# Kernel optimization log

Hardware: AMD Instinct MI355X
Metric: run time of the kernel (lower is better)

The kernel has to match this reference:

```python
import jax, jax.numpy as jnp
import numpy as np

KW = float(np.sqrt(3.0 * 3.0 / np.pi))  # hard-coded tube-of-response kernel width
EXT = 200.0  # half-extent of the FOV in mm (size = 400 per axis)
NLOR = 50000
NVOX = 128


def _make_lors(key, n, ext):
    # endpoints on opposite faces along the dominant (first) axis of the permuted frame
    k1, k2 = jax.random.split(key)
    yz1 = jax.random.uniform(k1, (2, n), minval=-ext, maxval=ext)
    yz2 = jax.random.uniform(k2, (2, n), minval=-ext, maxval=ext)
    x1 = jnp.full((1, n), -ext, jnp.float32)
    x2 = jnp.full((1, n), ext, jnp.float32)
    return jnp.concatenate([x1, yz1, x2, yz2], axis=0)  # [6, n]


def setup_inputs() -> dict:
    key = jax.random.key(0)
    ks = jax.random.split(key, 8)
    return {
        "image": jax.random.normal(ks[0], (NVOX, NVOX, NVOX), jnp.float32),
        "grid": jnp.array([NVOX, NVOX, NVOX], jnp.int32),
        "center": jnp.zeros((3,), jnp.float32),
        "size": jnp.full((3,), 2.0 * EXT, jnp.float32),
        "xlors": _make_lors(ks[1], NLOR, EXT),
        "ylors": _make_lors(ks[2], NLOR, EXT),
        "zlors": _make_lors(ks[3], NLOR, EXT),
        "xproj": jax.random.uniform(ks[4], (NLOR,), jnp.float32),
        "yproj": jax.random.uniform(ks[5], (NLOR,), jnp.float32),
        "zproj": jax.random.uniform(ks[6], (NLOR,), jnp.float32),
    }


def _backproject(shape, grid, center, size, lors, proj, kw):
    # Tube-of-response backprojection: march slices along axis 0, deposit a
    # Gaussian footprint (3x3 window) around the line crossing in each slice.
    N0, N1, N2 = shape
    v = size / grid.astype(jnp.float32)          # voxel size [3]
    lo = center - 0.5 * size                     # FOV lower corner [3]
    x = lo[0] + (jnp.arange(N0, dtype=jnp.float32) + 0.5) * v[0]  # slice centers [K]
    p1, p2 = lors[:, :3], lors[:, 3:6]           # [N,3]
    d = p2 - p1
    t = (x[None, :] - p1[:, :1]) / d[:, :1]      # [N,K]
    y = p1[:, 1:2] + t * d[:, 1:2]               # [N,K]
    z = p1[:, 2:3] + t * d[:, 2:3]
    fy = (y - lo[1]) / v[1] - 0.5                # fractional voxel coords
    fz = (z - lo[2]) / v[2] - 0.5
    off = jnp.arange(-1, 2)
    iy = jnp.floor(fy).astype(jnp.int32)[..., None] + off   # [N,K,3]
    iz = jnp.floor(fz).astype(jnp.int32)[..., None] + off
    cy = lo[1] + (iy.astype(jnp.float32) + 0.5) * v[1]
    cz = lo[2] + (iz.astype(jnp.float32) + 0.5) * v[2]
    dy = cy - y[..., None]
    dz = cz - z[..., None]
    d2 = dy[:, :, :, None] ** 2 + dz[:, :, None, :] ** 2    # [N,K,3,3]
    w = jnp.exp(-0.5 * d2 / (kw * kw))
    ok = ((iy >= 0) & (iy < N1))[:, :, :, None] \
       & ((iz >= 0) & (iz < N2))[:, :, None, :] \
       & ((t >= 0.0) & (t <= 1.0))[:, :, None, None]
    w = jnp.where(ok, w, 0.0) * proj[:, None, None, None]
    iyc = jnp.clip(iy, 0, N1 - 1)
    izc = jnp.clip(iz, 0, N2 - 1)
    kk = jnp.arange(N0)[None, :, None, None]
    flat = (kk * N1 + iyc[:, :, :, None]) * N2 + izc[:, :, None, :]  # [N,K,3,3]
    vol = jnp.zeros(N0 * N1 * N2, jnp.float32).at[flat.ravel()].add(w.ravel())
    return vol.reshape(N0, N1, N2)


def _perm(a, p):
    return a[jnp.array(p)]


def reference(image, grid, center, size, xlors, ylors, zlors, xproj, yproj, zproj):
    shape = image.shape
    # z-dominant LORs: base frame
    bpz = _backproject(shape, grid, center, size, zlors.T, zproj, KW)
    # x-dominant LORs: frame permuted [2,0,1], result transposed back [1,2,0]
    px = (2, 0, 1)
    shx = tuple(shape[i] for i in px)
    bpx = _backproject(shx, _perm(grid, px), _perm(center, px), _perm(size, px),
                       xlors.T, xproj, KW)
    bpxt = jnp.transpose(bpx, (1, 2, 0))
    # y-dominant LORs: frame permuted [1,0,2], result transposed back [1,0,2]
    py = (1, 0, 2)
    shy = tuple(shape[i] for i in py)
    bpy = _backproject(shy, _perm(grid, py), _perm(center, py), _perm(size, py),
                       ylors.T, yproj, KW)
    bpyt = jnp.transpose(bpy, (1, 0, 2))
    return bpxt + bpyt + bpz
```

## Files before the change

### kernel.cpp

```cpp
#include <hip/hip_runtime.h>
#include <stdint.h>

#define NVOX 128
#define VOL  (NVOX * NVOX * NVOX)
#define SLICE (NVOX * NVOX)
#define WPS  (SLICE / 2)
#define PVOL (VOL / 2)
#define NTHREADS 512
#define NREP 8
#define LO   (-200.0f)
#define VPIX 3.125f
#define INV_V 0.32f

#define NEGV2L (-2.4589628f)
#define NU_G   (4.9179256f)
#define NU_C   (2.4589628f)
#define C2     (0.0330793f)
#define FSCALE 1024.0f
#define INV_FSCALE (1.0f / 1024.0f)
#define MAGIC  12582912.0f

#define TROWS 132
#define TWORDS 66
#define TSZ (TROWS * TWORDS)

struct DepT {
    float wy0, wy1, wy2, wz0, wz1, wz2;
    int w0, sh;
};

__device__ __forceinline__ DepT dep_compute(float4 v, float prF, float t) {
    DepT d;
    float fy = fmaf(t, v.y, v.x);
    float fz = fmaf(t, v.w, v.z);
    float ffy = floorf(fy), ffz = floorf(fz);
    float gy = fy - ffy, hy = gy + 1.0f;
    d.wy0 = exp2f(NEGV2L * hy * hy) * prF;
    float uy = exp2f(fmaf(NU_G, gy, NU_C));
    d.wy1 = d.wy0 * uy;
    d.wy2 = d.wy1 * (uy * C2);
    float gz = fz - ffz, hz = gz + 1.0f;
    d.wz0 = exp2f(NEGV2L * hz * hz);
    float uz = exp2f(fmaf(NU_G, gz, NU_C));
    d.wz1 = d.wz0 * uz;
    d.wz2 = d.wz1 * (uz * C2);
    int row = (int)ffy + 1;
    int col = (int)ffz + 1;
    d.sh = (col & 1) << 4;
    d.w0 = row * TWORDS + (col >> 1);
    return d;
}

__device__ __forceinline__ void dep_fire(const DepT& d, unsigned* tile) {
    float wyc[3] = { d.wy0, d.wy1, d.wy2 };
    #pragma unroll
    for (int oy = 0; oy < 3; ++oy) {
        float w = wyc[oy];
        unsigned f0 = __float_as_uint(fmaf(w, d.wz0, MAGIC));
        unsigned f1 = __float_as_uint(fmaf(w, d.wz1, MAGIC));
        unsigned f2 = __float_as_uint(fmaf(w, d.wz2, MAGIC));
        unsigned lo = __builtin_amdgcn_perm(f1, f0, 0x05040100u);
        unsigned hi = f2 & 0xFFFFu;
        unsigned long long V = ((unsigned long long)hi << 32) | lo;
        V <<= d.sh;
        int b = d.w0 + oy * TWORDS;
        atomicAdd(&tile[b],     (unsigned)V);
        atomicAdd(&tile[b + 1], (unsigned)(V >> 32));
    }
}

__global__ __launch_bounds__(NTHREADS, 8) void bp_fused(
    const float4* __restrict__ pk,
    const float*  __restrict__ projF,
    unsigned* __restrict__ vols,
    int nlor)
{
    __shared__ unsigned tile[TSZ];
    const int k  = blockIdx.x;
    const int gy = blockIdx.y;
    const int dir   = (gy < 3) ? 0 : (gy < 6) ? 1 : 2;
    const int chunk = gy - dir * 3;
    const int nsd   = (dir == 2) ? 2 : 3;

    const float4* p   = pk + (size_t)dir * nlor;
    const float*  prf = projF + (size_t)dir * nlor;
    unsigned* vol = vols + (size_t)gy * PVOL;
    const int n0 = (int)(((long long)chunk * nlor) / nsd);
    const int n1 = (int)(((long long)(chunk + 1) * nlor) / nsd);

    for (int i = threadIdx.x; i < TSZ; i += NTHREADS) tile[i] = 0u;
    __syncthreads();

    const float t = (k + 0.5f) * 0.0078125f;

    int n = n0 + (int)threadIdx.x;
    for (; n + NTHREADS < n1; n += 2 * NTHREADS) {
        float4 vA = p[n];              float pA = prf[n];
        float4 vB = p[n + NTHREADS];   float pB = prf[n + NTHREADS];
        DepT dA = dep_compute(vA, pA, t);
        DepT dB = dep_compute(vB, pB, t);
        dep_fire(dA, tile);
        dep_fire(dB, tile);
    }
    if (n < n1) {
        DepT dA = dep_compute(p[n], prf[n], t);
        dep_fire(dA, tile);
    }
    __syncthreads();

    unsigned* dst = vol + (size_t)k * WPS;
    for (int i = threadIdx.x; i < WPS; i += NTHREADS) {
        int iy = i >> 6, w = i & 63;
        dst[i] = tile[(iy + 2) * TWORDS + w + 1];
    }
}

__global__ __launch_bounds__(256) void prep(
    const float* __restrict__ lz, const float* __restrict__ ly,
    const float* __restrict__ lx,
    const float* __restrict__ pz, const float* __restrict__ py,
    const float* __restrict__ px,
    float4* __restrict__ pk, float* __restrict__ projF, int nlor)
{
    int n = blockIdx.x * 256 + threadIdx.x;
    if (n >= nlor) return;
    const float* l  = (blockIdx.y == 0) ? lz : (blockIdx.y == 1) ? ly : lx;
    const float* pr = (blockIdx.y == 0) ? pz : (blockIdx.y == 1) ? py : px;
    float y1 = l[1 * nlor + n], z1 = l[2 * nlor + n];
    float y2 = l[4 * nlor + n], z2 = l[5 * nlor + n];
    pk[(size_t)blockIdx.y * nlor + n] =
        make_float4(fmaf(y1, INV_V, 63.5f), (y2 - y1) * INV_V,
                    fmaf(z1, INV_V, 63.5f), (z2 - z1) * INV_V);
    projF[(size_t)blockIdx.y * nlor + n] = pr[n] * FSCALE;
}

__global__ __launch_bounds__(256) void merge_all(
    float2* __restrict__ out, const unsigned* __restrict__ vols)
{
    __shared__ float T[64][65];
    const unsigned* vz = vols;
    const unsigned* vy = vols + 3 * (size_t)PVOL;
    const unsigned* vx = vols + 6 * (size_t)PVOL;
    int a  = blockIdx.x;
    int tb = (blockIdx.y & 1) * 64;
    int tc = (blockIdx.y >> 1) * 64;
    int wb = threadIdx.x & 31;
    int r0 = threadIdx.x >> 5;

    for (int cc = r0; cc < 64; cc += 8) {
        size_t wi = ((size_t)(tc + cc) * NVOX + a) * 64 + (tb >> 1) + wb;
        unsigned lo = 0, hi = 0;
        #pragma unroll
        for (int r = 0; r < 2; ++r) {
            unsigned w = vx[(size_t)r * PVOL + wi];
            lo += w & 0xFFFFu; hi += w >> 16;
        }
        T[cc][2 * wb]     = (float)lo * INV_FSCALE;
        T[cc][2 * wb + 1] = (float)hi * INV_FSCALE;
    }
    __syncthreads();
    for (int bb = r0; bb < 64; bb += 8) {
        int b = tb + bb;
        size_t zi = ((size_t)a * NVOX + b) * 64 + (tc >> 1) + wb;
        size_t yi = ((size_t)b * NVOX + a) * 64 + (tc >> 1) + wb;
        unsigned lo = 0, hi = 0;
        #pragma unroll
        for (int r = 0; r < 3; ++r) {
            unsigned wz = vz[(size_t)r * PVOL + zi];
            unsigned wy = vy[(size_t)r * PVOL + yi];
            lo += (wz & 0xFFFFu) + (wy & 0xFFFFu);
            hi += (wz >> 16) + (wy >> 16);
        }
        out[zi] = make_float2((float)lo * INV_FSCALE + T[2 * wb][bb],
                              (float)hi * INV_FSCALE + T[2 * wb + 1][bb]);
    }
}

template<int DIR>
__global__ __launch_bounds__(256) void bp_direct(
    const float* __restrict__ lors, const float* __restrict__ proj,
    float* __restrict__ out, int nlor)
{
    int tid = blockIdx.x * 256 + threadIdx.x;
    int k = tid & (NVOX - 1);
    int n = tid >> 7;
    if (n >= nlor) return;

    float p1x = lors[0 * nlor + n];
    float p1y = lors[1 * nlor + n];
    float p1z = lors[2 * nlor + n];
    float p2x = lors[3 * nlor + n];
    float p2y = lors[4 * nlor + n];
    float p2z = lors[5 * nlor + n];
    float pr  = proj[n];

    float xk = LO + (k + 0.5f) * VPIX;
    float t  = (xk - p1x) / (p2x - p1x);
    if (t < 0.0f || t > 1.0f) return;

    float y = p1y + t * (p2y - p1y);
    float z = p1z + t * (p2z - p1z);
    float fy = (y - LO) * INV_V - 0.5f;
    float fz = (z - LO) * INV_V - 0.5f;
    int iy0 = (int)floorf(fy) - 1;
    int iz0 = (int)floorf(fz) - 1;

    const float NEG = -0.17453292519943295f;
    float wy[3], wz[3];
    #pragma unroll
    for (int o = 0; o < 3; ++o) {
        int iy = iy0 + o;
        float dy = (iy + 0.5f) * VPIX + LO - y;
        wy[o] = (iy >= 0 && iy < NVOX) ? __expf(NEG * dy * dy) * pr : 0.0f;
        int iz = iz0 + o;
        float dz = (iz + 0.5f) * VPIX + LO - z;
        wz[o] = (iz >= 0 && iz < NVOX) ? __expf(NEG * dz * dz) : 0.0f;
    }
    #pragma unroll
    for (int oy = 0; oy < 3; ++oy) {
        if (wy[oy] == 0.0f) continue;
        int iy = iy0 + oy;
        #pragma unroll
        for (int oz = 0; oz < 3; ++oz) {
            if (wz[oz] == 0.0f) continue;
            int iz = iz0 + oz;
            int idx = (DIR == 0) ? (iy * NVOX + iz) * NVOX + k
                    : (DIR == 1) ? (iy * NVOX + k) * NVOX + iz
                                 : (k * NVOX + iy) * NVOX + iz;
            atomicAdd(&out[idx], wy[oy] * wz[oz]);
        }
    }
}

extern "C" void kernel_launch(void* const* d_in, const int* in_sizes, int n_in,
                              void* d_out, int out_size, void* d_ws, size_t ws_size,
                              hipStream_t stream) {
    const float* xlors = (const float*)d_in[4];
    const float* ylors = (const float*)d_in[5];
    const float* zlors = (const float*)d_in[6];
    const float* xproj = (const float*)d_in[7];
    const float* yproj = (const float*)d_in[8];
    const float* zproj = (const float*)d_in[9];
    float* out = (float*)d_out;
    const int nlor = in_sizes[7];
    const size_t volsB = (size_t)NREP * PVOL * sizeof(unsigned);
    const size_t pkB   = 3 * (size_t)nlor * sizeof(float4);
    const size_t pfB   = 3 * (size_t)nlor * sizeof(float);

    if (ws_size >= volsB + pkB + pfB && (nlor & 1) == 0) {
        unsigned* vols = (unsigned*)d_ws;
        float4* pkv   = (float4*)((char*)d_ws + volsB);
        float*  projF = (float*)((char*)d_ws + volsB + pkB);

        dim3 pgrid((nlor + 255) / 256, 3);
        prep<<<pgrid, 256, 0, stream>>>(zlors, ylors, xlors,
                                        zproj, yproj, xproj, pkv, projF, nlor);

        dim3 bgrid(NVOX, NREP);
        bp_fused<<<bgrid, NTHREADS, 0, stream>>>(pkv, projF, vols, nlor);

        dim3 mgrid(NVOX, 4);
        merge_all<<<mgrid, 256, 0, stream>>>((float2*)out, vols);
    } else {
        hipMemsetAsync(d_out, 0, (size_t)VOL * sizeof(float), stream);
        const int blocks = (nlor * NVOX + 255) / 256;
        bp_direct<0><<<blocks, 256, 0, stream>>>(xlors, xproj, out, nlor);
        bp_direct<1><<<blocks, 256, 0, stream>>>(ylors, yproj, out, nlor);
        bp_direct<2><<<blocks, 256, 0, stream>>>(zlors, zproj, out, nlor);
    }
}
```

Before: 60.44 us.

## Pack row pairs into 64-bit LDS words to halve shared atomics per deposit

Changes the shared-memory tile layout so that each 64-bit word holds two adjacent rows' packed 16-bit accumulators. Each 3x3 footprint now takes four 64-bit LDS atomic adds instead of six 32-bit ones, with parity-dependent select logic to place the rows. The tile grows slightly (66x66 u64), which may affect occupancy. Carries between the packed 16-bit fields must stay within each 32-bit half, which relies on the existing headroom.

```diff
diff --git a/kernel.cpp b/kernel.cpp
--- a/kernel.cpp
+++ b/kernel.cpp
@@ -20,13 +20,12 @@
 #define INV_FSCALE (1.0f / 1024.0f)
 #define MAGIC  12582912.0f
 
-#define TROWS 132
-#define TWORDS 66
-#define TSZ (TROWS * TWORDS)
+#define QW 66
+#define QSZ (QW * QW)
 
 struct DepT {
     float wy0, wy1, wy2, wz0, wz1, wz2;
-    int w0, sh;
+    int qb, sh, ry;
 };
 
 __device__ __forceinline__ DepT dep_compute(float4 v, float prF, float t) {
@@ -47,12 +46,14 @@
     int row = (int)ffy + 1;
     int col = (int)ffz + 1;
     d.sh = (col & 1) << 4;
-    d.w0 = row * TWORDS + (col >> 1);
+    d.ry = row & 1;
+    d.qb = (row >> 1) * QW + (col >> 1);
     return d;
 }
 
-__device__ __forceinline__ void dep_fire(const DepT& d, unsigned* tile) {
+__device__ __forceinline__ void dep_fire(const DepT& d, unsigned long long* qt) {
     float wyc[3] = { d.wy0, d.wy1, d.wy2 };
+    unsigned l[3], h[3];
     #pragma unroll
     for (int oy = 0; oy < 3; ++oy) {
         float w = wyc[oy];
@@ -63,10 +64,18 @@
         unsigned hi = f2 & 0xFFFFu;
         unsigned long long V = ((unsigned long long)hi << 32) | lo;
         V <<= d.sh;
-        int b = d.w0 + oy * TWORDS;
-        atomicAdd(&tile[b],     (unsigned)V);
-        atomicAdd(&tile[b + 1], (unsigned)(V >> 32));
-    }
+        l[oy] = (unsigned)V;
+        h[oy] = (unsigned)(V >> 32);
+    }
+    bool o = (d.ry != 0);
+    unsigned tA = o ? 0u   : l[0], tB = o ? l[0] : l[1];
+    unsigned tC = o ? 0u   : h[0], tD = o ? h[0] : h[1];
+    unsigned bA = o ? l[1] : l[2], bB = o ? l[2] : 0u;
+    unsigned bC = o ? h[1] : h[2], bD = o ? h[2] : 0u;
+    atomicAdd(&qt[d.qb],          tA | ((unsigned long long)tB << 32));
+    atomicAdd(&qt[d.qb + 1],      tC | ((unsigned long long)tD << 32));
+    atomicAdd(&qt[d.qb + QW],     bA | ((unsigned long long)bB << 32));
+    atomicAdd(&qt[d.qb + QW + 1], bC | ((unsigned long long)bD << 32));
 }
 
 __global__ __launch_bounds__(NTHREADS, 8) void bp_fused(
@@ -75,7 +84,7 @@
     unsigned* __restrict__ vols,
     int nlor)
 {
-    __shared__ unsigned tile[TSZ];
+    __shared__ unsigned long long qtile[QSZ];
     const int k  = blockIdx.x;
     const int gy = blockIdx.y;
     const int dir   = (gy < 3) ? 0 : (gy < 6) ? 1 : 2;
@@ -88,7 +97,7 @@
     const int n0 = (int)(((long long)chunk * nlor) / nsd);
     const int n1 = (int)(((long long)(chunk + 1) * nlor) / nsd);
 
-    for (int i = threadIdx.x; i < TSZ; i += NTHREADS) tile[i] = 0u;
+    for (int i = threadIdx.x; i < QSZ; i += NTHREADS) qtile[i] = 0ull;
     __syncthreads();
 
     const float t = (k + 0.5f) * 0.0078125f;
@@ -99,19 +108,21 @@
         float4 vB = p[n + NTHREADS];   float pB = prf[n + NTHREADS];
         DepT dA = dep_compute(vA, pA, t);
         DepT dB = dep_compute(vB, pB, t);
-        dep_fire(dA, tile);
-        dep_fire(dB, tile);
+        dep_fire(dA, qtile);
+        dep_fire(dB, qtile);
     }
     if (n < n1) {
         DepT dA = dep_compute(p[n], prf[n], t);
-        dep_fire(dA, tile);
+        dep_fire(dA, qtile);
     }
     __syncthreads();
 
     unsigned* dst = vol + (size_t)k * WPS;
     for (int i = threadIdx.x; i < WPS; i += NTHREADS) {
         int iy = i >> 6, w = i & 63;
-        dst[i] = tile[(iy + 2) * TWORDS + w + 1];
+        int row = iy + 2;
+        unsigned long long q = qtile[(row >> 1) * QW + (w + 1)];
+        dst[i] = (row & 1) ? (unsigned)(q >> 32) : (unsigned)q;
     }
 }
 
```

New measurement: 65.38 us. 8.2% more time.
